# Kernel optimization log

Hardware: AMD Instinct MI355X
Metric: run time of the kernel (lower is better)

Reference implementation:

```python
import jax, jax.numpy as jnp
import numpy as np

N_NODES = 50000
N_EDGES = 1600000
NFEAT = 128
NHID = 128
NCLASS = 64
BATCH = 8


def setup_inputs() -> dict:
    key = jax.random.key(0)
    ks = jax.random.split(key, 8)
    x = jax.random.normal(ks[0], (BATCH, N_NODES, NFEAT), dtype=jnp.float32)
    edge_rows = jnp.sort(jax.random.randint(ks[1], (N_EDGES,), 0, N_NODES))
    edge_cols = jax.random.randint(ks[2], (N_EDGES,), 0, N_NODES)
    # roughly degree-normalized positive weights (avg degree 32)
    edge_vals = jax.random.uniform(ks[3], (N_EDGES,), dtype=jnp.float32) / 32.0
    s1 = 1.0 / np.sqrt(NFEAT)
    W1 = jax.random.normal(ks[4], (NFEAT, NHID), dtype=jnp.float32) * s1
    W2 = jax.random.normal(ks[5], (NHID, NHID), dtype=jnp.float32) * s1
    W3 = jax.random.normal(ks[6], (NHID, NCLASS), dtype=jnp.float32) * s1
    b1 = jnp.zeros((NHID,), dtype=jnp.float32)
    b2 = jnp.zeros((NHID,), dtype=jnp.float32)
    b3 = jnp.zeros((NCLASS,), dtype=jnp.float32)
    return {"x": x, "edge_rows": edge_rows, "edge_cols": edge_cols,
            "edge_vals": edge_vals, "W1": W1, "b1": b1, "W2": W2,
            "b2": b2, "W3": W3, "b3": b3}


def _gcn_layer(x, W, b, rows, cols, vals, n_nodes):
    """Batched SPGraphConvolution: spmm(adj, x @ W) + b, x: [B, N, d_in]."""
    support = jnp.einsum("bnd,de->bne", x, W)  # [B, N, d_out]

    def spmm(s):  # s: [N, d_out]
        msgs = s[cols] * vals[:, None]  # gather + scale, [E, d_out]
        return jax.ops.segment_sum(msgs, rows, num_segments=n_nodes)

    return jax.vmap(spmm)(support) + b


def reference(x, edge_rows, edge_cols, edge_vals, W1, b1, W2, b2, W3, b3):
    n = x.shape[1]
    # dropout in eval mode (training=False) for determinism
    h = jax.nn.relu(_gcn_layer(x, W1, b1, edge_rows, edge_cols, edge_vals, n) + x)
    h = jax.nn.relu(_gcn_layer(h, W2, b2, edge_rows, edge_cols, edge_vals, n) + h)
    h = jax.nn.relu(_gcn_layer(h, W3, b3, edge_rows, edge_cols, edge_vals, n))
    return jax.nn.sigmoid(h)
```

## Files before the change

### kernel.cpp

```cpp
#include <hip/hip_runtime.h>

constexpr int NN = 50000;
constexpr int NE = 1600000;
constexpr int NB = 8;
constexpr int M_ROWS = NN * NB;

typedef unsigned short ushort;
typedef unsigned int uint;
typedef unsigned char uchar;
typedef float f32x2v __attribute__((ext_vector_type(2)));
typedef float f32x4v __attribute__((ext_vector_type(4)));
typedef uint u32x4 __attribute__((ext_vector_type(4)));
typedef uint u32x2 __attribute__((ext_vector_type(2)));

__device__ __forceinline__ ushort f2bf(float f) {
  union { float f; uint u; } v;
  v.f = f;
  const uint r = v.u + 0x7fffu + ((v.u >> 16) & 1u);
  return (ushort)(r >> 16);
}
__device__ __forceinline__ float bfhi(uint g) {
  union { uint u; float f; } v;
  v.u = g & 0xffff0000u;
  return v.f;
}
__device__ __forceinline__ float bflo(uint g) {
  union { uint u; float f; } v;
  v.u = g << 16;
  return v.f;
}

__device__ __forceinline__ void fp8x4_to_f32(uint v, float& a, float& b,
                                             float& c, float& d) {
#if __has_builtin(__builtin_amdgcn_cvt_pk_f32_fp8)
  const f32x2v lo = __builtin_amdgcn_cvt_pk_f32_fp8((int)v, false);
  const f32x2v hi = __builtin_amdgcn_cvt_pk_f32_fp8((int)v, true);
  a = lo.x; b = lo.y; c = hi.x; d = hi.y;
#else
  union { _Float16 h; ushort u; } c0, c1, c2, c3;
  c0.u = (ushort)(((v & 0x80u) << 8) | ((v & 0x7fu) << 7));
  c1.u = (ushort)(((v & 0x8000u)) | ((v & 0x7f00u) >> 1));
  c2.u = (ushort)(((v >> 16) & 0x8000u ? 0x8000u : 0u) |
                  (((v >> 16) & 0x7fu) << 7));
  c3.u = (ushort)((((v >> 24) & 0x80u) << 8) | (((v >> 24) & 0x7fu) << 7));
  c2.u = (ushort)((((v >> 16) & 0x80u) << 8) | (((v >> 16) & 0x7fu) << 7));
  a = (float)c0.h * 256.0f;
  b = (float)c1.h * 256.0f;
  c = (float)c2.h * 256.0f;
  d = (float)c3.h * 256.0f;
#endif
}
__device__ __forceinline__ uint f32_to_fp8(float x) {
#if __has_builtin(__builtin_amdgcn_cvt_pk_fp8_f32)
  return (uint)__builtin_amdgcn_cvt_pk_fp8_f32(x, x, 0, false) & 0xffu;
#else
  union { _Float16 h; ushort u; } c;
  c.h = (_Float16)(x * (1.0f / 256.0f));
  const uint h = c.u;
  uint r = h & 0x7fffu;
  r = (r + 0x3Fu + ((r >> 7) & 1u)) >> 7;
  if (r > 0x7Eu) r = 0x7Eu;
  return ((h >> 8) & 0x80u) | r;
#endif
}

__global__ __launch_bounds__(256) void rowptr_kernel(const int* __restrict__ rows,
                                                     int* __restrict__ row_ptr) {
  const int r = blockIdx.x * 256 + threadIdx.x;
  if (r > NN) return;
  int lo = 0, hi = NE;
  while (lo < hi) {
    const int mid = (lo + hi) >> 1;
    if (rows[mid] < r) lo = mid + 1;
    else hi = mid;
  }
  row_ptr[r] = lo;
}

__global__ __launch_bounds__(256) void wtrans_kernel(const float* __restrict__ W,
                                                     ushort* __restrict__ Wt,
                                                     int dout) {
  const int idx = blockIdx.x * 256 + threadIdx.x;
  if (idx >= dout * 128) return;
  const int n = idx >> 7;
  const int k = idx & 127;
  Wt[idx] = f2bf(W[k * dout + n]);
}

template <int DOUT, bool ABF16>
__global__ __launch_bounds__(256) void gemm_mfma(const void* __restrict__ Av,
                                                 const ushort* __restrict__ Wt,
                                                 uchar* __restrict__ S) {
  constexpr int PACK = 256 / DOUT;
  constexpr int NT = DOUT / 16;
  constexpr int LDK = 136;
  constexpr int LB = DOUT + 16;
  typedef __attribute__((ext_vector_type(8))) short bf16x8;
  typedef __attribute__((ext_vector_type(4))) float f32x4;

  __shared__ ushort As[64 * LDK];
  __shared__ ushort Ws[DOUT * LDK];

  const int t = threadIdx.x;
  const int w = t >> 6;
  const int l = t & 63;
  const size_t m0 = (size_t)blockIdx.x * 64;

  if constexpr (ABF16) {
    const ushort* A = (const ushort*)Av;
#pragma unroll
    for (int q = 0; q < 4; q++) {
      const int chunk = t + q * 256;
      const int row = chunk >> 4;
      const int off = (chunk & 15) * 8;
      *(u32x4*)(As + row * LDK + off) =
          __builtin_nontemporal_load((const u32x4*)(A + (m0 + row) * 128 + off));
    }
  } else {
    const float* A = (const float*)Av;
    const int row = t >> 2;
    const int c0 = (t & 3) * 32;
    const float* src = A + (m0 + row) * 128 + c0;
    ushort* dst = As + row * LDK + c0;
#pragma unroll
    for (int q = 0; q < 8; q++) {
      const f32x4v g = __builtin_nontemporal_load((const f32x4v*)(src + q * 4));
      dst[q * 4 + 0] = f2bf(g.x);
      dst[q * 4 + 1] = f2bf(g.y);
      dst[q * 4 + 2] = f2bf(g.z);
      dst[q * 4 + 3] = f2bf(g.w);
    }
  }
  {
#pragma unroll
    for (int q = 0; q < (DOUT * 128) / (8 * 256); q++) {
      const int chunk = t + q * 256;
      const int n = chunk >> 4;
      const int off = (chunk & 15) * 8;
      *(uint4*)(Ws + n * LDK + off) = *(const uint4*)(Wt + n * 128 + off);
    }
  }
  __syncthreads();

  const int mrow = w * 16 + (l & 15);
  const int q8 = (l >> 4) * 8;

  bf16x8 a[4];
  const ushort* ap = As + mrow * LDK + q8;
#pragma unroll
  for (int ks = 0; ks < 4; ks++) a[ks] = *(const bf16x8*)(ap + ks * 32);

  f32x4 acc[NT];
#pragma unroll
  for (int nt = 0; nt < NT; nt++) acc[nt] = (f32x4)0.f;

#pragma unroll
  for (int nt = 0; nt < NT; nt++) {
    const ushort* bp = Ws + (nt * 16 + (l & 15)) * LDK + q8;
#pragma unroll
    for (int ks = 0; ks < 4; ks++) {
      const bf16x8 b = *(const bf16x8*)(bp + ks * 32);
      acc[nt] = __builtin_amdgcn_mfma_f32_16x16x32_bf16(a[ks], b, acc[nt], 0, 0, 0);
    }
  }

  __syncthreads();
  uchar* Ab = (uchar*)As;
  const int erow = w * 16 + (l >> 4) * 4;
  const int ecol = l & 15;
#pragma unroll
  for (int nt = 0; nt < NT; nt++)
#pragma unroll
    for (int r = 0; r < 4; r++)
      Ab[(erow + r) * LB + nt * 16 + ecol] = (uchar)f32_to_fp8(acc[nt][r]);
  __syncthreads();

#pragma unroll
  for (int q = 0; q < (64 * DOUT) / (16 * 256); q++) {
    const int chunk = t + q * 256;
    const int row = chunk / (DOUT / 16);
    const int off = (chunk % (DOUT / 16)) * 16;
    const uint4 v = *(const uint4*)(Ab + row * LB + off);
    const int m = (int)m0 + row;
    const int b = m / NN;
    const int n = m - b * NN;
    *(uint4*)(S + ((size_t)(b / PACK) * NN + n) * 256 + (b % PACK) * DOUT + off) = v;
  }
}

template <int PACK, int RMODE, bool SIGMOID, bool OBF16>
__global__ __launch_bounds__(256) void spmm_kernel(
    const uchar* __restrict__ S, const int* __restrict__ row_ptr,
    const int* __restrict__ cols, const float* __restrict__ vals,
    const float* __restrict__ bias, const void* resid, void* out) {
  constexpr int DOUT = 256 / PACK;
  constexpr int LPB = 64 / PACK;

  const int wave = threadIdx.x >> 6;
  const int lane = threadIdx.x & 63;
  const int r = blockIdx.x * 4 + wave;
  const int bg = lane / LPB;
  const int j = (lane % LPB) * 4;
  const int b = blockIdx.y * PACK + bg;
  const uchar* Sb = S + (size_t)blockIdx.y * NN * 256 + lane * 4;

  float a0 = 0.f, a1 = 0.f, a2 = 0.f, a3 = 0.f;

  const int e0 = row_ptr[r];
  const int e1 = row_ptr[r + 1];

  for (int e = e0; e < e1; e += 64) {
    const int n = min(64, e1 - e);
    int c = 0;
    float wv = 0.f;
    if (lane < n) {
      c = __builtin_nontemporal_load(cols + e + lane);
      wv = __builtin_nontemporal_load(vals + e + lane);
    }
    int i = 0;
    for (; i + 8 <= n; i += 8) {
      int cc[8];
      float ww[8];
      uint gg[8];
#pragma unroll
      for (int s = 0; s < 8; s++) {
        cc[s] = __shfl(c, i + s);
        ww[s] = __shfl(wv, i + s);
      }
#pragma unroll
      for (int s = 0; s < 8; s++)
        gg[s] = *(const uint*)(Sb + (size_t)cc[s] * 256);
#pragma unroll
      for (int s = 0; s < 8; s++) {
        float v0, v1, v2, v3;
        fp8x4_to_f32(gg[s], v0, v1, v2, v3);
        a0 += ww[s] * v0;
        a1 += ww[s] * v1;
        a2 += ww[s] * v2;
        a3 += ww[s] * v3;
      }
    }
    for (; i < n; i++) {
      const int ci = __shfl(c, i);
      const float wi = __shfl(wv, i);
      const uint g = *(const uint*)(Sb + (size_t)ci * 256);
      float v0, v1, v2, v3;
      fp8x4_to_f32(g, v0, v1, v2, v3);
      a0 += wi * v0;
      a1 += wi * v1;
      a2 += wi * v2;
      a3 += wi * v3;
    }
  }

  const size_t orow = (size_t)(b * NN + r) * DOUT + j;
  const f32x4v bb = *(const f32x4v*)(bias + j);
  a0 += bb.x;
  a1 += bb.y;
  a2 += bb.z;
  a3 += bb.w;
  if constexpr (RMODE == 1) {
    const f32x4v res =
        __builtin_nontemporal_load((const f32x4v*)((const float*)resid + orow));
    a0 += res.x;
    a1 += res.y;
    a2 += res.z;
    a3 += res.w;
  } else if constexpr (RMODE == 2) {
    const u32x2 g =
        __builtin_nontemporal_load((const u32x2*)((const ushort*)resid + orow));
    a0 += bflo(g.x);
    a1 += bfhi(g.x);
    a2 += bflo(g.y);
    a3 += bfhi(g.y);
  }
  a0 = fmaxf(a0, 0.f);
  a1 = fmaxf(a1, 0.f);
  a2 = fmaxf(a2, 0.f);
  a3 = fmaxf(a3, 0.f);
  if constexpr (SIGMOID) {
    a0 = 1.f / (1.f + __expf(-a0));
    a1 = 1.f / (1.f + __expf(-a1));
    a2 = 1.f / (1.f + __expf(-a2));
    a3 = 1.f / (1.f + __expf(-a3));
  }
  if constexpr (OBF16) {
    u32x2 o;
    o.x = (uint)f2bf(a0) | ((uint)f2bf(a1) << 16);
    o.y = (uint)f2bf(a2) | ((uint)f2bf(a3) << 16);
    __builtin_nontemporal_store(o, (u32x2*)((ushort*)out + orow));
  } else {
    f32x4v o;
    o.x = a0;
    o.y = a1;
    o.z = a2;
    o.w = a3;
    __builtin_nontemporal_store(o, (f32x4v*)((float*)out + orow));
  }
}

extern "C" void kernel_launch(void* const* d_in, const int* in_sizes, int n_in,
                              void* d_out, int out_size, void* d_ws, size_t ws_size,
                              hipStream_t stream) {
  const float* x = (const float*)d_in[0];
  const int* erows = (const int*)d_in[1];
  const int* ecols = (const int*)d_in[2];
  const float* evals = (const float*)d_in[3];
  const float* W1 = (const float*)d_in[4];
  const float* b1 = (const float*)d_in[5];
  const float* W2 = (const float*)d_in[6];
  const float* b2 = (const float*)d_in[7];
  const float* W3 = (const float*)d_in[8];
  const float* b3 = (const float*)d_in[9];

  char* ws = (char*)d_ws;
  int* row_ptr = (int*)ws;
  ushort* Wt1 = (ushort*)(ws + 0x40000);
  ushort* Wt2 = (ushort*)(ws + 0x48000);
  ushort* Wt3 = (ushort*)(ws + 0x50000);
  uchar* Sf8 = (uchar*)(ws + 0x60000);
  ushort* H = (ushort*)(ws + 0x60000 + (size_t)M_ROWS * 128);

  rowptr_kernel<<<(NN + 256) / 256, 256, 0, stream>>>(erows, row_ptr);
  wtrans_kernel<<<(128 * 128) / 256, 256, 0, stream>>>(W1, Wt1, 128);
  wtrans_kernel<<<(128 * 128) / 256, 256, 0, stream>>>(W2, Wt2, 128);
  wtrans_kernel<<<(64 * 128) / 256, 256, 0, stream>>>(W3, Wt3, 64);

  const dim3 sgrid128(NN / 4, NB / 2);
  const dim3 sgrid64(NN / 4, NB / 4);

  gemm_mfma<128, false><<<M_ROWS / 64, 256, 0, stream>>>(x, Wt1, Sf8);
  spmm_kernel<2, 1, false, true><<<sgrid128, 256, 0, stream>>>(
      Sf8, row_ptr, ecols, evals, b1, x, H);
  gemm_mfma<128, true><<<M_ROWS / 64, 256, 0, stream>>>(H, Wt2, Sf8);
  spmm_kernel<2, 2, false, true><<<sgrid128, 256, 0, stream>>>(
      Sf8, row_ptr, ecols, evals, b2, H, H);
  gemm_mfma<64, true><<<M_ROWS / 64, 256, 0, stream>>>(H, Wt3, Sf8);
  spmm_kernel<4, 0, true, false><<<sgrid64, 256, 0, stream>>>(
      Sf8, row_ptr, ecols, evals, b3, nullptr, (float*)d_out);
}
```

Before: 984.1 us.

## Read GEMM weights from global, widen SpMM gather unroll, use packed FMA

The GEMM kernel stops staging the transposed weight matrix in shared memory. It reads B fragments directly from global/L2, which frees LDS and may raise occupancy, and it packs the bf16 conversions of A into wider LDS stores. The SpMM kernel pre-shifts column indices into 32-bit byte offsets and interleaves shuffles with gathers in 16-wide batches, adding a 4-wide tail. It also accumulates with packed two-wide FMAs on the fp8-converted pairs. The risks are more global traffic per GEMM block and higher register pressure from the 16-deep gather batch, and the 32-bit offset math assumes each batch slice fits in 4 GB.

```diff
diff --git a/kernel.cpp b/kernel.cpp
--- a/kernel.cpp
+++ b/kernel.cpp
@@ -30,24 +30,20 @@
   return v.f;
 }
 
-__device__ __forceinline__ void fp8x4_to_f32(uint v, float& a, float& b,
-                                             float& c, float& d) {
+__device__ __forceinline__ void fp8x4_to_f32x2(uint v, f32x2v& lo, f32x2v& hi) {
 #if __has_builtin(__builtin_amdgcn_cvt_pk_f32_fp8)
-  const f32x2v lo = __builtin_amdgcn_cvt_pk_f32_fp8((int)v, false);
-  const f32x2v hi = __builtin_amdgcn_cvt_pk_f32_fp8((int)v, true);
-  a = lo.x; b = lo.y; c = hi.x; d = hi.y;
+  lo = __builtin_amdgcn_cvt_pk_f32_fp8((int)v, false);
+  hi = __builtin_amdgcn_cvt_pk_f32_fp8((int)v, true);
 #else
   union { _Float16 h; ushort u; } c0, c1, c2, c3;
   c0.u = (ushort)(((v & 0x80u) << 8) | ((v & 0x7fu) << 7));
   c1.u = (ushort)(((v & 0x8000u)) | ((v & 0x7f00u) >> 1));
-  c2.u = (ushort)(((v >> 16) & 0x8000u ? 0x8000u : 0u) |
-                  (((v >> 16) & 0x7fu) << 7));
+  c2.u = (ushort)((((v >> 16) & 0x80u) << 8) | (((v >> 16) & 0x7fu) << 7));
   c3.u = (ushort)((((v >> 24) & 0x80u) << 8) | (((v >> 24) & 0x7fu) << 7));
-  c2.u = (ushort)((((v >> 16) & 0x80u) << 8) | (((v >> 16) & 0x7fu) << 7));
-  a = (float)c0.h * 256.0f;
-  b = (float)c1.h * 256.0f;
-  c = (float)c2.h * 256.0f;
-  d = (float)c3.h * 256.0f;
+  lo.x = (float)c0.h * 256.0f;
+  lo.y = (float)c1.h * 256.0f;
+  hi.x = (float)c2.h * 256.0f;
+  hi.y = (float)c3.h * 256.0f;
 #endif
 }
 __device__ __forceinline__ uint f32_to_fp8(float x) {
@@ -99,7 +95,6 @@
   typedef __attribute__((ext_vector_type(4))) float f32x4;
 
   __shared__ ushort As[64 * LDK];
-  __shared__ ushort Ws[DOUT * LDK];
 
   const int t = threadIdx.x;
   const int w = t >> 6;
@@ -125,19 +120,10 @@
 #pragma unroll
     for (int q = 0; q < 8; q++) {
       const f32x4v g = __builtin_nontemporal_load((const f32x4v*)(src + q * 4));
-      dst[q * 4 + 0] = f2bf(g.x);
-      dst[q * 4 + 1] = f2bf(g.y);
-      dst[q * 4 + 2] = f2bf(g.z);
-      dst[q * 4 + 3] = f2bf(g.w);
-    }
-  }
-  {
-#pragma unroll
-    for (int q = 0; q < (DOUT * 128) / (8 * 256); q++) {
-      const int chunk = t + q * 256;
-      const int n = chunk >> 4;
-      const int off = (chunk & 15) * 8;
-      *(uint4*)(Ws + n * LDK + off) = *(const uint4*)(Wt + n * 128 + off);
+      u32x2 p;
+      p.x = (uint)f2bf(g.x) | ((uint)f2bf(g.y) << 16);
+      p.y = (uint)f2bf(g.z) | ((uint)f2bf(g.w) << 16);
+      *(u32x2*)(dst + q * 4) = p;
     }
   }
   __syncthreads();
@@ -154,9 +140,10 @@
 #pragma unroll
   for (int nt = 0; nt < NT; nt++) acc[nt] = (f32x4)0.f;
 
+  const ushort* wp = Wt + (l & 15) * 128 + q8;
 #pragma unroll
   for (int nt = 0; nt < NT; nt++) {
-    const ushort* bp = Ws + (nt * 16 + (l & 15)) * LDK + q8;
+    const ushort* bp = wp + nt * 16 * 128;
 #pragma unroll
     for (int ks = 0; ks < 4; ks++) {
       const bf16x8 b = *(const bf16x8*)(bp + ks * 32);
@@ -202,56 +189,73 @@
   const int bg = lane / LPB;
   const int j = (lane % LPB) * 4;
   const int b = blockIdx.y * PACK + bg;
-  const uchar* Sb = S + (size_t)blockIdx.y * NN * 256 + lane * 4;
-
-  float a0 = 0.f, a1 = 0.f, a2 = 0.f, a3 = 0.f;
+  const uchar* __restrict__ Sg = S + (size_t)blockIdx.y * ((size_t)NN * 256);
+  const uint lane4 = (uint)lane << 2;
+
+  f32x2v a01 = {0.f, 0.f};
+  f32x2v a23 = {0.f, 0.f};
 
   const int e0 = row_ptr[r];
   const int e1 = row_ptr[r + 1];
 
   for (int e = e0; e < e1; e += 64) {
     const int n = min(64, e1 - e);
-    int c = 0;
+    uint c8 = 0;
     float wv = 0.f;
     if (lane < n) {
-      c = __builtin_nontemporal_load(cols + e + lane);
+      c8 = (uint)__builtin_nontemporal_load(cols + e + lane) << 8;
       wv = __builtin_nontemporal_load(vals + e + lane);
     }
     int i = 0;
-    for (; i + 8 <= n; i += 8) {
-      int cc[8];
-      float ww[8];
-      uint gg[8];
-#pragma unroll
-      for (int s = 0; s < 8; s++) {
-        cc[s] = __shfl(c, i + s);
+    for (; i + 16 <= n; i += 16) {
+      float ww[16];
+      uint gg[16];
+#pragma unroll
+      for (int s = 0; s < 16; s++) {
+        const uint off = (uint)__shfl((int)c8, i + s) + lane4;
         ww[s] = __shfl(wv, i + s);
+        gg[s] = *(const uint*)(Sg + off);
       }
 #pragma unroll
-      for (int s = 0; s < 8; s++)
-        gg[s] = *(const uint*)(Sb + (size_t)cc[s] * 256);
-#pragma unroll
-      for (int s = 0; s < 8; s++) {
-        float v0, v1, v2, v3;
-        fp8x4_to_f32(gg[s], v0, v1, v2, v3);
-        a0 += ww[s] * v0;
-        a1 += ww[s] * v1;
-        a2 += ww[s] * v2;
-        a3 += ww[s] * v3;
+      for (int s = 0; s < 16; s++) {
+        f32x2v lo, hi;
+        fp8x4_to_f32x2(gg[s], lo, hi);
+        const f32x2v w2 = {ww[s], ww[s]};
+        a01 = __builtin_elementwise_fma(w2, lo, a01);
+        a23 = __builtin_elementwise_fma(w2, hi, a23);
       }
     }
+    for (; i + 4 <= n; i += 4) {
+      float ww[4];
+      uint gg[4];
+#pragma unroll
+      for (int s = 0; s < 4; s++) {
+        const uint off = (uint)__shfl((int)c8, i + s) + lane4;
+        ww[s] = __shfl(wv, i + s);
+        gg[s] = *(const uint*)(Sg + off);
+      }
+#pragma unroll
+      for (int s = 0; s < 4; s++) {
+        f32x2v lo, hi;
+        fp8x4_to_f32x2(gg[s], lo, hi);
+        const f32x2v w2 = {ww[s], ww[s]};
+        a01 = __builtin_elementwise_fma(w2, lo, a01);
+        a23 = __builtin_elementwise_fma(w2, hi, a23);
+      }
+    }
     for (; i < n; i++) {
-      const int ci = __shfl(c, i);
+      const uint off = (uint)__shfl((int)c8, i) + lane4;
       const float wi = __shfl(wv, i);
-      const uint g = *(const uint*)(Sb + (size_t)ci * 256);
-      float v0, v1, v2, v3;
-      fp8x4_to_f32(g, v0, v1, v2, v3);
-      a0 += wi * v0;
-      a1 += wi * v1;
-      a2 += wi * v2;
-      a3 += wi * v3;
-    }
-  }
+      const uint g = *(const uint*)(Sg + off);
+      f32x2v lo, hi;
+      fp8x4_to_f32x2(g, lo, hi);
+      const f32x2v w2 = {wi, wi};
+      a01 = __builtin_elementwise_fma(w2, lo, a01);
+      a23 = __builtin_elementwise_fma(w2, hi, a23);
+    }
+  }
+
+  float a0 = a01.x, a1 = a01.y, a2 = a23.x, a3 = a23.y;
 
   const size_t orow = (size_t)(b * NN + r) * DOUT + j;
   const f32x4v bb = *(const f32x4v*)(bias + j);
```

Measured after the change: 1.102 ms. +12.0%, slower.
